# Optimization experiments

Measured on AMD Instinct MI355X. Metric: run time of the kernel, lower is better.

The kernel has to match this reference:

```python
import jax, jax.numpy as jnp
import numpy as np

N_NODES = 50000
N_EDGES = 500000
N_GRAPHS = 64
IN_DIM = 64
HID = 128
N_LAYERS = 2
BN_EPS = 1e-5


def setup_inputs() -> dict:
    key = jax.random.key(0)
    ks = jax.random.split(key, 12)
    x = jax.random.normal(ks[0], (N_NODES, IN_DIM), dtype=jnp.float32)
    edge_index = jax.random.randint(ks[1], (2, N_EDGES), 0, N_NODES, dtype=jnp.int64)
    batch = jnp.sort(jax.random.randint(ks[2], (N_NODES,), 0, N_GRAPHS, dtype=jnp.int64))
    s = 0.05
    W_enc = jax.random.normal(ks[3], (IN_DIM, HID), dtype=jnp.float32) * s
    b_enc = jnp.zeros((HID,), dtype=jnp.float32)
    Wc = jax.random.normal(ks[4], (N_LAYERS, HID, HID), dtype=jnp.float32) * s
    bc = jnp.zeros((N_LAYERS, HID), dtype=jnp.float32)
    gamma = jnp.ones((N_LAYERS, HID), dtype=jnp.float32)
    beta = jnp.zeros((N_LAYERS, HID), dtype=jnp.float32)
    MID = HID // 2
    W1 = jax.random.normal(ks[5], (HID, MID), dtype=jnp.float32) * s
    b1 = jnp.zeros((MID,), dtype=jnp.float32)
    W2 = jax.random.normal(ks[6], (MID, 1), dtype=jnp.float32) * s
    b2 = jnp.zeros((1,), dtype=jnp.float32)
    return {"x": x, "edge_index": edge_index, "batch": batch,
            "W_enc": W_enc, "b_enc": b_enc, "Wc": Wc, "bc": bc,
            "gamma": gamma, "beta": beta, "W1": W1, "b1": b1,
            "W2": W2, "b2": b2}


def _gcn_conv(h, src, dst, norm, W, b, n_nodes):
    # h: [N, HID]; src/dst: [E+N] (self-loops included); norm: [E+N]
    h = h @ W                                   # [N, HID]
    msg = h[src] * norm[:, None]                # gather + normalize
    out = jax.ops.segment_sum(msg, dst, num_segments=n_nodes)  # scatter-add
    return out + b


def _batch_norm(h, g, b):
    mu = jnp.mean(h, axis=0)
    var = jnp.var(h, axis=0)
    return (h - mu) * jax.lax.rsqrt(var + BN_EPS) * g + b


def reference(x, edge_index, batch, W_enc, b_enc, Wc, bc, gamma, beta, W1, b1, W2, b2):
    n = x.shape[0]
    loop = jnp.arange(n, dtype=edge_index.dtype)
    src = jnp.concatenate([edge_index[0], loop])   # [E+N]
    dst = jnp.concatenate([edge_index[1], loop])
    # symmetric GCN normalization with self-loops: deg over target index
    deg = jax.ops.segment_sum(jnp.ones_like(dst, dtype=x.dtype), dst, num_segments=n)
    dinv = jax.lax.rsqrt(deg)                      # deg >= 1 due to self-loops
    norm = dinv[src] * dinv[dst]                   # [E+N]

    h = x @ W_enc + b_enc                          # node encoder
    for l in range(Wc.shape[0]):
        h = _gcn_conv(h, src, dst, norm, Wc[l], bc[l], n)
        h = _batch_norm(h, gamma[l], beta[l])
        h = jax.nn.relu(h)                         # dropout inactive (eval)

    # global mean pool over graphs
    pooled = jax.ops.segment_sum(h, batch, num_segments=N_GRAPHS)
    counts = jax.ops.segment_sum(jnp.ones((n,), dtype=h.dtype), batch, num_segments=N_GRAPHS)
    pooled = pooled / jnp.maximum(counts, 1.0)[:, None]

    z = jax.nn.relu(pooled @ W1 + b1)
    out = jax.nn.sigmoid(z @ W2 + b2)              # [B, 1]
    return out.squeeze(-1)                          # [B]
```

## Files before the change

### kernel.cpp

```cpp
#include <hip/hip_runtime.h>
#include <hip/hip_bf16.h>
#include <hip/hip_fp16.h>
#include <math.h>


typedef _Float16 f16x8 __attribute__((ext_vector_type(8)));
typedef float f32x4 __attribute__((ext_vector_type(4)));

__device__ inline unsigned pack2(float a, float b) {
  union { __half2 h; unsigned u; } p;
  p.h = __floats2half2_rn(a, b);
  return p.u;
}
__device__ inline float2 unpack2(unsigned u) {
  union { unsigned u; __half2 h; } p;
  p.u = u;
  return __half22float2(p.h);
}

__global__ __launch_bounds__(256) void k_setup(
    int* __restrict__ deg, float* __restrict__ bnstat, int statTotal,
    float* __restrict__ pooled, int N, int nbN,
    const float* __restrict__ W_enc, const float* __restrict__ b_enc,
    const float* __restrict__ Wc, unsigned short* __restrict__ MT,
    float* __restrict__ bfold, int NL,
    const float* __restrict__ Wc1, unsigned short* __restrict__ WT1,
    const int* __restrict__ batch, int* __restrict__ gstart) {
  int b = blockIdx.x;
  if (b < nbN) {
    int i = b * 256 + threadIdx.x;
    if (i < N) deg[i] = 1;
    if (i < statTotal) bnstat[i] = 0.f;
    if (i < 64 * 128) pooled[i] = 0.f;
    return;
  }
  b -= nbN;
  if (b < 65) {
    if (threadIdx.x < 128) {
      int n = threadIdx.x;
      int k = b;
      const float* arow = (k < 64) ? (W_enc + (size_t)k * 128) : b_enc;
      float acc = 0.f;
      for (int j = 0; j < 128; j++)
        acc = fmaf(arow[j], Wc[(size_t)j * 128 + n], acc);
      if (k < 64) ((__half*)MT)[(size_t)n * 64 + k] = __float2half(acc);
      else bfold[n] = acc;
    }
    return;
  }
  b -= 65;
  if (b < 64) {
    if (NL > 1) {
      int i = b * 256 + threadIdx.x;
      int n = i & 127, k = i >> 7;
      ((__half*)WT1)[(size_t)n * 128 + k] = __float2half(Wc1[i]);
    }
    return;
  }
  int g = threadIdx.x;
  if (g <= 64) {
    int lo = 0, hi = N;
    while (lo < hi) {
      int mid = (lo + hi) >> 1;
      if (batch[mid] < g) lo = mid + 1;
      else hi = mid;
    }
    gstart[g] = lo;
  }
}

__global__ __launch_bounds__(256) void k_deg(const int* __restrict__ ei, int E,
                                             int* __restrict__ deg) {
  int i = blockIdx.x * 256 + threadIdx.x;
  if (i < E) atomicAdd(&deg[ei[E + i]], 1);
}

__global__ __launch_bounds__(256) void k_scan_a(const int* __restrict__ deg, int N,
                                                int* __restrict__ rowptr,
                                                int* __restrict__ blksum) {
  __shared__ int s[256];
  int t = threadIdx.x;
  int i = blockIdx.x * 256 + t;
  int v = (i < N) ? deg[i] : 0;
  s[t] = v;
  __syncthreads();
  for (int off = 1; off < 256; off <<= 1) {
    int x = (t >= off) ? s[t - off] : 0;
    __syncthreads();
    s[t] += x;
    __syncthreads();
  }
  if (i < N) rowptr[i] = s[t] - v;
  if (t == 255) blksum[blockIdx.x] = s[255];
}

__global__ __launch_bounds__(256) void k_scan_c(const int* __restrict__ deg, int N,
                                                int total,
                                                const int* __restrict__ blksum,
                                                int* __restrict__ rowptr,
                                                int* __restrict__ cursor,
                                                float* __restrict__ dinv) {
  __shared__ int red[256];
  int t = threadIdx.x, b = blockIdx.x;
  int acc = 0;
  for (int j = t; j < b; j += 256) acc += blksum[j];
  red[t] = acc;
  __syncthreads();
  for (int off = 128; off > 0; off >>= 1) {
    if (t < off) red[t] += red[t + off];
    __syncthreads();
  }
  int prefix = red[0];
  int i = b * 256 + t;
  if (i < N) {
    int rp = rowptr[i] + prefix;
    rowptr[i] = rp;
    cursor[i] = rp;
    dinv[i] = rsqrtf((float)deg[i]);
  } else if (i == N) {
    rowptr[N] = total;
  }
}

__global__ __launch_bounds__(256) void k_fillprep(
    const int* __restrict__ ei, int E, int N, int nbEN,
    int* __restrict__ cursor, int* __restrict__ colx,
    const float* __restrict__ x, const float* __restrict__ dinv,
    unsigned* __restrict__ xs2) {
  int b = blockIdx.x;
  if (b < nbEN) {
    int i = b * 256 + threadIdx.x;
    if (i < E) {
      int s = ei[i];
      int d = ei[E + i];
      int pos = atomicAdd(&cursor[d], 1);
      colx[pos] = s;
    } else if (i < E + N) {
      int j = i - E;
      int pos = atomicAdd(&cursor[j], 1);
      colx[pos] = j;
    }
    return;
  }
  b -= nbEN;
  int i = b * 256 + threadIdx.x;
  if (i < N * 16) {
    int row = i >> 4;
    float4 v = ((const float4*)x)[i];
    float d = dinv[row];
    uint2 o;
    o.x = pack2(v.x * d, v.y * d);
    o.y = pack2(v.z * d, v.w * d);
    ((uint2*)xs2)[i] = o;
  }
}

__global__ __launch_bounds__(256, 2) void k_aggemm0(
    const uint2* __restrict__ xs, const int* __restrict__ rowptr,
    const int* __restrict__ colx, const float* __restrict__ dinv,
    const unsigned short* __restrict__ MT,
    const float* __restrict__ bias,
    const float* __restrict__ bias2,
    float* __restrict__ stat,
    unsigned short* __restrict__ Yh, int N) {
  constexpr int KP = 68;
  __shared__ unsigned short Al[64 * KP];
  __shared__ float wvl[64];
  __shared__ float red[4][2][128];

  int lane = threadIdx.x & 63;
  int wv = threadIdx.x >> 6;
  int grp = lane >> 4, l16 = lane & 15;
  int rowBlk = blockIdx.x * 64;

#pragma unroll 1
  for (int it = 0; it < 4; it++) {
    int lr = it * 16 + wv * 4 + grp;
    int i = rowBlk + lr;
    float s0 = 0.f, s1 = 0.f, s2 = 0.f, s3 = 0.f, sd = 0.f;
    if (i < N) {
      int beg = rowptr[i], end = rowptr[i + 1];
      int e = beg;
#pragma unroll 1
      for (; e + 8 <= end; e += 8) {
        int ix[8];
#pragma unroll
        for (int u = 0; u < 8; u++) ix[u] = colx[e + u];
        uint2 v[8];
        float dd[8];
#pragma unroll
        for (int u = 0; u < 8; u++) { v[u] = xs[(size_t)ix[u] * 16 + l16]; dd[u] = dinv[ix[u]]; }
#pragma unroll
        for (int u = 0; u < 8; u++) {
          float2 a = unpack2(v[u].x), b = unpack2(v[u].y);
          s0 += a.x; s1 += a.y; s2 += b.x; s3 += b.y;
          sd += dd[u];
        }
      }
#pragma unroll 1
      for (; e < end; e++) {
        int sr = colx[e];
        uint2 vv = xs[(size_t)sr * 16 + l16];
        float2 a = unpack2(vv.x), b = unpack2(vv.y);
        s0 += a.x; s1 += a.y; s2 += b.x; s3 += b.y;
        sd += dinv[sr];
      }
    }
    float di = (i < N) ? dinv[i] : 0.f;
    *(uint2*)&Al[lr * KP + l16 * 4] =
        make_uint2(pack2(s0 * di, s1 * di), pack2(s2 * di, s3 * di));
    if (l16 == 0) wvl[lr] = di * sd;
  }
  __syncthreads();

  int l15 = lane & 15;
  int kg = lane >> 4;
  f16x8 af[2];
#pragma unroll
  for (int j = 0; j < 2; j++)
    af[j] = *(const f16x8*)&Al[(wv * 16 + l15) * KP + kg * 8 + j * 32];

  f32x4 acc[8];
#pragma unroll
  for (int t = 0; t < 8; t++) acc[t] = {0.f, 0.f, 0.f, 0.f};
#pragma unroll
  for (int j = 0; j < 2; j++) {
#pragma unroll
    for (int t = 0; t < 8; t++) {
      f16x8 bf = *(const f16x8*)&MT[(size_t)(t * 16 + l15) * 64 + kg * 8 + j * 32];
      acc[t] = __builtin_amdgcn_mfma_f32_16x16x32_f16(af[j], bf, acc[t], 0, 0, 0);
    }
  }

  int rbaseL = wv * 16 + kg * 4;
  int rbase = rowBlk + rbaseL;
  float wrow[4];
#pragma unroll
  for (int r = 0; r < 4; r++) wrow[r] = wvl[rbaseL + r];

#pragma unroll
  for (int t = 0; t < 8; t++) {
    int ch = t * 16 + l15;
    float bb = bias[ch];
    float b2v = bias2[ch];
    float s = 0.f, q = 0.f;
#pragma unroll
    for (int r = 0; r < 4; r++) {
      int row = rbase + r;
      if (row < N) {
        float o = fmaf(wrow[r], b2v, acc[t][r] + bb);
        __half oh = __float2half(o);
        Yh[(size_t)row * 128 + ch] = *(unsigned short*)&oh;
        s += o;
        q += o * o;
      }
    }
    s += __shfl_xor(s, 16); s += __shfl_xor(s, 32);
    q += __shfl_xor(q, 16); q += __shfl_xor(q, 32);
    if (kg == 0) { red[wv][0][ch] = s; red[wv][1][ch] = q; }
  }
  __syncthreads();
  int st = threadIdx.x >> 7, ch2 = threadIdx.x & 127;
  float v = red[0][st][ch2] + red[1][st][ch2] + red[2][st][ch2] + red[3][st][ch2];
  atomicAdd(&stat[(blockIdx.x & 7) * 256 + st * 128 + ch2], v);
}

__global__ __launch_bounds__(256, 2) void k_aggemm1(
    const unsigned short* __restrict__ Hprev,
    const int* __restrict__ rowptr, const int* __restrict__ colx,
    const float* __restrict__ dinv,
    const unsigned short* __restrict__ WT,
    const float* __restrict__ statPrev, const float* __restrict__ gamma,
    const float* __restrict__ beta, float invN,
    const float* __restrict__ bias,
    float* __restrict__ statCur, unsigned short* __restrict__ Yh, int N) {
  constexpr int KP = 136;
  __shared__ unsigned short Al[64 * KP];
  __shared__ float scsh[256];
  __shared__ float red[4][2][128];

  if (threadIdx.x < 128) {
    int c = threadIdx.x;
    float ss = 0.f, qs = 0.f;
#pragma unroll
    for (int r = 0; r < 8; r++) {
      ss += statPrev[r * 256 + c];
      qs += statPrev[r * 256 + 128 + c];
    }
    float mu = ss * invN;
    float var = qs * invN - mu * mu;
    float sc = rsqrtf(var + 1e-5f) * gamma[c];
    scsh[c] = sc;
    scsh[128 + c] = beta[c] - mu * sc;
  }
  __syncthreads();

  int lane = threadIdx.x & 63;
  int wv = threadIdx.x >> 6;
  int half = lane >> 5, l32 = lane & 31;
  int rowBlk = blockIdx.x * 64;
  const uint2* Hp = (const uint2*)Hprev;
  float4 sc = ((const float4*)scsh)[l32];
  float4 sh = ((const float4*)(scsh + 128))[l32];

#pragma unroll 1
  for (int it = 0; it < 8; it++) {
    int lr = it * 8 + wv * 2 + half;
    int i = rowBlk + lr;
    float4 s = make_float4(0.f, 0.f, 0.f, 0.f);
    if (i < N) {
      int beg = rowptr[i], end = rowptr[i + 1];
      int e = beg;
#pragma unroll 1
      for (; e + 4 <= end; e += 4) {
        int i0 = colx[e + 0], i1 = colx[e + 1], i2 = colx[e + 2], i3 = colx[e + 3];
        uint2 v0 = Hp[(size_t)i0 * 32 + l32];
        uint2 v1 = Hp[(size_t)i1 * 32 + l32];
        uint2 v2 = Hp[(size_t)i2 * 32 + l32];
        uint2 v3 = Hp[(size_t)i3 * 32 + l32];
        float d0 = dinv[i0], d1 = dinv[i1], d2 = dinv[i2], d3 = dinv[i3];
        float2 a, b;
        a = unpack2(v0.x); b = unpack2(v0.y);
        s.x += fmaxf(fmaf(a.x, sc.x, sh.x), 0.f) * d0;
        s.y += fmaxf(fmaf(a.y, sc.y, sh.y), 0.f) * d0;
        s.z += fmaxf(fmaf(b.x, sc.z, sh.z), 0.f) * d0;
        s.w += fmaxf(fmaf(b.y, sc.w, sh.w), 0.f) * d0;
        a = unpack2(v1.x); b = unpack2(v1.y);
        s.x += fmaxf(fmaf(a.x, sc.x, sh.x), 0.f) * d1;
        s.y += fmaxf(fmaf(a.y, sc.y, sh.y), 0.f) * d1;
        s.z += fmaxf(fmaf(b.x, sc.z, sh.z), 0.f) * d1;
        s.w += fmaxf(fmaf(b.y, sc.w, sh.w), 0.f) * d1;
        a = unpack2(v2.x); b = unpack2(v2.y);
        s.x += fmaxf(fmaf(a.x, sc.x, sh.x), 0.f) * d2;
        s.y += fmaxf(fmaf(a.y, sc.y, sh.y), 0.f) * d2;
        s.z += fmaxf(fmaf(b.x, sc.z, sh.z), 0.f) * d2;
        s.w += fmaxf(fmaf(b.y, sc.w, sh.w), 0.f) * d2;
        a = unpack2(v3.x); b = unpack2(v3.y);
        s.x += fmaxf(fmaf(a.x, sc.x, sh.x), 0.f) * d3;
        s.y += fmaxf(fmaf(a.y, sc.y, sh.y), 0.f) * d3;
        s.z += fmaxf(fmaf(b.x, sc.z, sh.z), 0.f) * d3;
        s.w += fmaxf(fmaf(b.y, sc.w, sh.w), 0.f) * d3;
      }
#pragma unroll 1
      for (; e < end; e++) {
        int sr = colx[e];
        uint2 vv = Hp[(size_t)sr * 32 + l32];
        float dsr = dinv[sr];
        float2 a = unpack2(vv.x), b = unpack2(vv.y);
        s.x += fmaxf(fmaf(a.x, sc.x, sh.x), 0.f) * dsr;
        s.y += fmaxf(fmaf(a.y, sc.y, sh.y), 0.f) * dsr;
        s.z += fmaxf(fmaf(b.x, sc.z, sh.z), 0.f) * dsr;
        s.w += fmaxf(fmaf(b.y, sc.w, sh.w), 0.f) * dsr;
      }
    }
    float di = (i < N) ? dinv[i] : 0.f;
    *(uint2*)&Al[lr * KP + l32 * 4] =
        make_uint2(pack2(s.x * di, s.y * di), pack2(s.z * di, s.w * di));
  }
  __syncthreads();

  int l15 = lane & 15;
  int kg = lane >> 4;
  f16x8 af[4];
#pragma unroll
  for (int j = 0; j < 4; j++)
    af[j] = *(const f16x8*)&Al[(wv * 16 + l15) * KP + kg * 8 + j * 32];

  f32x4 acc[8];
#pragma unroll
  for (int t = 0; t < 8; t++) acc[t] = {0.f, 0.f, 0.f, 0.f};
#pragma unroll
  for (int j = 0; j < 4; j++) {
#pragma unroll
    for (int t = 0; t < 8; t++) {
      f16x8 bf = *(const f16x8*)&WT[(size_t)(t * 16 + l15) * 128 + kg * 8 + j * 32];
      acc[t] = __builtin_amdgcn_mfma_f32_16x16x32_f16(af[j], bf, acc[t], 0, 0, 0);
    }
  }

  int rbase = rowBlk + wv * 16 + kg * 4;
#pragma unroll
  for (int t = 0; t < 8; t++) {
    int ch = t * 16 + l15;
    float bb = bias[ch];
    float s = 0.f, q = 0.f;
#pragma unroll
    for (int r = 0; r < 4; r++) {
      int row = rbase + r;
      if (row < N) {
        float o = acc[t][r] + bb;
        __half oh = __float2half(o);
        Yh[(size_t)row * 128 + ch] = *(unsigned short*)&oh;
        s += o;
        q += o * o;
      }
    }
    s += __shfl_xor(s, 16); s += __shfl_xor(s, 32);
    q += __shfl_xor(q, 16); q += __shfl_xor(q, 32);
    if (kg == 0) { red[wv][0][ch] = s; red[wv][1][ch] = q; }
  }
  __syncthreads();
  int st = threadIdx.x >> 7, ch2 = threadIdx.x & 127;
  float v = red[0][st][ch2] + red[1][st][ch2] + red[2][st][ch2] + red[3][st][ch2];
  atomicAdd(&statCur[(blockIdx.x & 7) * 256 + st * 128 + ch2], v);
}

__global__ __launch_bounds__(256) void k_wprep(const float* __restrict__ Wsrc,
                                               unsigned short* __restrict__ WT) {
  int i = blockIdx.x * 256 + threadIdx.x;
  int n = i & 127, k = i >> 7;
  ((__half*)WT)[(size_t)n * 128 + k] = __float2half(Wsrc[i]);
}

__global__ __launch_bounds__(256) void k_pool(
    const unsigned* __restrict__ H16u,
    const float* __restrict__ stat, const float* __restrict__ gamma,
    const float* __restrict__ beta, float invN,
    const int* __restrict__ gstart, float* __restrict__ pooled) {
  __shared__ float scsh[256];
  __shared__ float red[4][128];
  if (threadIdx.x < 128) {
    int c = threadIdx.x;
    float ss = 0.f, qs = 0.f;
#pragma unroll
    for (int r = 0; r < 8; r++) {
      ss += stat[r * 256 + c];
      qs += stat[r * 256 + 128 + c];
    }
    float mu = ss * invN;
    float var = qs * invN - mu * mu;
    float sc = rsqrtf(var + 1e-5f) * gamma[c];
    scsh[c] = sc;
    scsh[128 + c] = beta[c] - mu * sc;
  }
  __syncthreads();

  int g = blockIdx.x >> 3;
  int part = blockIdx.x & 7;
  int beg = gstart[g], end = gstart[g + 1];
  int len = end - beg;
  int p0 = beg + (len * part) / 8;
  int p1 = beg + (len * (part + 1)) / 8;

  int l64 = threadIdx.x & 63;
  int rs = threadIdx.x >> 6;
  int c0 = l64 * 2;
  float sc0 = scsh[c0], sc1 = scsh[c0 + 1];
  float sh0 = scsh[128 + c0], sh1 = scsh[128 + c0 + 1];
  int plen = p1 - p0;
  int q0 = p0 + (plen * rs) / 4;
  int q1 = p0 + (plen * (rs + 1)) / 4;

  float a0 = 0.f, a1 = 0.f;
  for (int r = q0; r < q1; r++) {
    float2 f = unpack2(H16u[(size_t)r * 64 + l64]);
    a0 += fmaxf(fmaf(f.x, sc0, sh0), 0.f);
    a1 += fmaxf(fmaf(f.y, sc1, sh1), 0.f);
  }
  red[rs][c0] = a0;
  red[rs][c0 + 1] = a1;
  __syncthreads();
  if (threadIdx.x < 128) {
    float s = red[0][threadIdx.x] + red[1][threadIdx.x] +
              red[2][threadIdx.x] + red[3][threadIdx.x];
    atomicAdd(&pooled[g * 128 + threadIdx.x], s);
  }
}

__global__ __launch_bounds__(256) void k_mlp(const float* __restrict__ pooled,
                                             const int* __restrict__ gstart,
                                             const float* __restrict__ W1,
                                             const float* __restrict__ b1,
                                             const float* __restrict__ W2,
                                             const float* __restrict__ b2,
                                             float* __restrict__ out) {
  __shared__ float P[64 * 128];
  __shared__ float Z[64 * 64];
  for (int i = threadIdx.x; i < 64 * 128; i += 256) {
    int g = i >> 7;
    int cnt = gstart[g + 1] - gstart[g];
    P[i] = pooled[i] / (float)(cnt > 1 ? cnt : 1);
  }
  __syncthreads();
  for (int i = threadIdx.x; i < 64 * 64; i += 256) {
    int g = i >> 6, m = i & 63;
    float acc = b1[m];
    for (int k = 0; k < 128; k++) acc += P[(g << 7) + k] * W1[k * 64 + m];
    Z[i] = fmaxf(acc, 0.f);
  }
  __syncthreads();
  if (threadIdx.x < 64) {
    int g = threadIdx.x;
    float acc = b2[0];
    for (int m = 0; m < 64; m++) acc += Z[(g << 6) + m] * W2[m];
    out[g] = 1.f / (1.f + expf(-acc));
  }
}


extern "C" void kernel_launch(void* const* d_in, const int* in_sizes, int n_in,
                              void* d_out, int out_size, void* d_ws, size_t ws_size,
                              hipStream_t stream) {
  const float* x      = (const float*)d_in[0];
  const int*   ei     = (const int*)d_in[1];
  const int*   batch  = (const int*)d_in[2];
  const float* W_enc  = (const float*)d_in[3];
  const float* b_enc  = (const float*)d_in[4];
  const float* Wc     = (const float*)d_in[5];
  const float* bc     = (const float*)d_in[6];
  const float* gamma  = (const float*)d_in[7];
  const float* beta   = (const float*)d_in[8];
  const float* W1     = (const float*)d_in[9];
  const float* b1     = (const float*)d_in[10];
  const float* W2     = (const float*)d_in[11];
  const float* b2     = (const float*)d_in[12];
  float* out = (float*)d_out;

  const int N = in_sizes[2];
  const int E = in_sizes[1] / 2;
  const int NL = in_sizes[6] / 128;

  size_t off = 0;
  auto alloc = [&](size_t bytes) {
    void* p = (char*)d_ws + off;
    off += (bytes + 255) & ~(size_t)255;
    return p;
  };
  unsigned short* h16a = (unsigned short*)alloc((size_t)N * 128 * 2);
  unsigned short* h16b = (unsigned short*)alloc((size_t)N * 128 * 2);
  int*   deg    = (int*)alloc((size_t)N * 4);
  float* dinv   = (float*)alloc((size_t)N * 4);
  int*   rowptr = (int*)alloc((size_t)(N + 1) * 4);
  int*   cursor = (int*)alloc((size_t)N * 4);
  int*   colx   = (int*)alloc((size_t)(E + N) * 4);
  int*   blksum = (int*)alloc(1024 * 4);
  float* bnstat = (float*)alloc((size_t)NL * 2048 * 4);
  float* pooled = (float*)alloc(64 * 128 * 4);
  int*   gstart = (int*)alloc(65 * 4);
  unsigned short* MT  = (unsigned short*)alloc(128 * 64 * 2);
  unsigned short* WT1 = (unsigned short*)alloc(128 * 128 * 2);
  float* bfold  = (float*)alloc(128 * 4);
  unsigned* xs  = (unsigned*)alloc((size_t)N * 64 * 2);

  int nbN = (N + 255) / 256;
  int nbEN = (E + N + 255) / 256;
  float invN = 1.f / (float)N;
  int tiles = (N + 63) / 64;

  k_setup<<<nbN + 130, 256, 0, stream>>>(
      deg, bnstat, NL * 2048, pooled, N, nbN, W_enc, b_enc, Wc, MT, bfold, NL,
      Wc + (size_t)128 * 128, WT1, batch, gstart);
  k_deg<<<(E + 255) / 256, 256, 0, stream>>>(ei, E, deg);
  k_scan_a<<<nbN, 256, 0, stream>>>(deg, N, rowptr, blksum);
  k_scan_c<<<nbN, 256, 0, stream>>>(deg, N, E + N, blksum, rowptr, cursor, dinv);
  k_fillprep<<<nbEN + (N * 16 + 255) / 256, 256, 0, stream>>>(
      ei, E, N, nbEN, cursor, colx, x, dinv, xs);

  k_aggemm0<<<tiles, 256, 0, stream>>>((const uint2*)xs, rowptr, colx, dinv,
                                       MT, bc, bfold, bnstat, h16a, N);

  unsigned short* cur = h16a;
  unsigned short* nxt = h16b;
  for (int l = 1; l < NL; l++) {
    if (l > 1)
      k_wprep<<<64, 256, 0, stream>>>(Wc + (size_t)l * 128 * 128, WT1);
    k_aggemm1<<<tiles, 256, 0, stream>>>(
        cur, rowptr, colx, dinv, WT1, bnstat + (l - 1) * 2048,
        gamma + (l - 1) * 128, beta + (l - 1) * 128, invN, bc + l * 128,
        bnstat + l * 2048, nxt, N);
    unsigned short* tmp = cur; cur = nxt; nxt = tmp;
  }

  k_pool<<<64 * 8, 256, 0, stream>>>((const unsigned*)cur,
                                     bnstat + (NL - 1) * 2048,
                                     gamma + (NL - 1) * 128,
                                     beta + (NL - 1) * 128, invN, gstart,
                                     pooled);
  k_mlp<<<1, 256, 0, stream>>>(pooled, gstart, W1, b1, W2, b2, out);
}
```

Measured before the change: 282.7 us.

## Halve row tiles to 32, split GEMM over 2x2 waves, unroll gather by 8

Both fused aggregate+GEMM kernels now process 32 rows per block instead of 64. The four waves split the MFMA output as 2 row-halves by 2 column-halves, so each wave keeps 4 accumulators instead of 8. Launch bounds are raised to 4 blocks per SM to allow more waves in flight for the latency-bound neighbor gather. The layer-1 gather loop is unrolled to 8 edges for more memory-level parallelism. The grid doubles, which adds more per-block BN-stat atomics and more redundant weight-fragment reads per row.

After: 258.5 us. -8.6%, faster.

```diff
diff --git a/kernel.cpp b/kernel.cpp
--- a/kernel.cpp
+++ b/kernel.cpp
@@ -155,7 +155,7 @@
   }
 }
 
-__global__ __launch_bounds__(256, 2) void k_aggemm0(
+__global__ __launch_bounds__(256, 4) void k_aggemm0(
     const uint2* __restrict__ xs, const int* __restrict__ rowptr,
     const int* __restrict__ colx, const float* __restrict__ dinv,
     const unsigned short* __restrict__ MT,
@@ -164,17 +164,17 @@
     float* __restrict__ stat,
     unsigned short* __restrict__ Yh, int N) {
   constexpr int KP = 68;
-  __shared__ unsigned short Al[64 * KP];
-  __shared__ float wvl[64];
-  __shared__ float red[4][2][128];
+  __shared__ unsigned short Al[32 * KP];
+  __shared__ float wvl[32];
+  __shared__ float red[2][2][128];
 
   int lane = threadIdx.x & 63;
   int wv = threadIdx.x >> 6;
   int grp = lane >> 4, l16 = lane & 15;
-  int rowBlk = blockIdx.x * 64;
+  int rowBlk = blockIdx.x * 32;
 
 #pragma unroll 1
-  for (int it = 0; it < 4; it++) {
+  for (int it = 0; it < 2; it++) {
     int lr = it * 16 + wv * 4 + grp;
     int i = rowBlk + lr;
     float s0 = 0.f, s1 = 0.f, s2 = 0.f, s3 = 0.f, sd = 0.f;
@@ -215,32 +215,33 @@
 
   int l15 = lane & 15;
   int kg = lane >> 4;
+  int wr = wv & 1, wc = wv >> 1;
   f16x8 af[2];
 #pragma unroll
   for (int j = 0; j < 2; j++)
-    af[j] = *(const f16x8*)&Al[(wv * 16 + l15) * KP + kg * 8 + j * 32];
-
-  f32x4 acc[8];
-#pragma unroll
-  for (int t = 0; t < 8; t++) acc[t] = {0.f, 0.f, 0.f, 0.f};
+    af[j] = *(const f16x8*)&Al[(wr * 16 + l15) * KP + kg * 8 + j * 32];
+
+  f32x4 acc[4];
+#pragma unroll
+  for (int t = 0; t < 4; t++) acc[t] = {0.f, 0.f, 0.f, 0.f};
 #pragma unroll
   for (int j = 0; j < 2; j++) {
 #pragma unroll
-    for (int t = 0; t < 8; t++) {
-      f16x8 bf = *(const f16x8*)&MT[(size_t)(t * 16 + l15) * 64 + kg * 8 + j * 32];
+    for (int t = 0; t < 4; t++) {
+      f16x8 bf = *(const f16x8*)&MT[(size_t)(wc * 64 + t * 16 + l15) * 64 + kg * 8 + j * 32];
       acc[t] = __builtin_amdgcn_mfma_f32_16x16x32_f16(af[j], bf, acc[t], 0, 0, 0);
     }
   }
 
-  int rbaseL = wv * 16 + kg * 4;
+  int rbaseL = wr * 16 + kg * 4;
   int rbase = rowBlk + rbaseL;
   float wrow[4];
 #pragma unroll
   for (int r = 0; r < 4; r++) wrow[r] = wvl[rbaseL + r];
 
 #pragma unroll
-  for (int t = 0; t < 8; t++) {
-    int ch = t * 16 + l15;
+  for (int t = 0; t < 4; t++) {
+    int ch = wc * 64 + t * 16 + l15;
     float bb = bias[ch];
     float b2v = bias2[ch];
     float s = 0.f, q = 0.f;
@@ -257,15 +258,15 @@
     }
     s += __shfl_xor(s, 16); s += __shfl_xor(s, 32);
     q += __shfl_xor(q, 16); q += __shfl_xor(q, 32);
-    if (kg == 0) { red[wv][0][ch] = s; red[wv][1][ch] = q; }
+    if (kg == 0) { red[wr][0][ch] = s; red[wr][1][ch] = q; }
   }
   __syncthreads();
   int st = threadIdx.x >> 7, ch2 = threadIdx.x & 127;
-  float v = red[0][st][ch2] + red[1][st][ch2] + red[2][st][ch2] + red[3][st][ch2];
+  float v = red[0][st][ch2] + red[1][st][ch2];
   atomicAdd(&stat[(blockIdx.x & 7) * 256 + st * 128 + ch2], v);
 }
 
-__global__ __launch_bounds__(256, 2) void k_aggemm1(
+__global__ __launch_bounds__(256, 4) void k_aggemm1(
     const unsigned short* __restrict__ Hprev,
     const int* __restrict__ rowptr, const int* __restrict__ colx,
     const float* __restrict__ dinv,
@@ -275,9 +276,9 @@
     const float* __restrict__ bias,
     float* __restrict__ statCur, unsigned short* __restrict__ Yh, int N) {
   constexpr int KP = 136;
-  __shared__ unsigned short Al[64 * KP];
+  __shared__ unsigned short Al[32 * KP];
   __shared__ float scsh[256];
-  __shared__ float red[4][2][128];
+  __shared__ float red[2][2][128];
 
   if (threadIdx.x < 128) {
     int c = threadIdx.x;
@@ -298,13 +299,13 @@
   int lane = threadIdx.x & 63;
   int wv = threadIdx.x >> 6;
   int half = lane >> 5, l32 = lane & 31;
-  int rowBlk = blockIdx.x * 64;
+  int rowBlk = blockIdx.x * 32;
   const uint2* Hp = (const uint2*)Hprev;
   float4 sc = ((const float4*)scsh)[l32];
   float4 sh = ((const float4*)(scsh + 128))[l32];
 
 #pragma unroll 1
-  for (int it = 0; it < 8; it++) {
+  for (int it = 0; it < 4; it++) {
     int lr = it * 8 + wv * 2 + half;
     int i = rowBlk + lr;
     float4 s = make_float4(0.f, 0.f, 0.f, 0.f);
@@ -312,34 +313,22 @@
       int beg = rowptr[i], end = rowptr[i + 1];
       int e = beg;
 #pragma unroll 1
-      for (; e + 4 <= end; e += 4) {
-        int i0 = colx[e + 0], i1 = colx[e + 1], i2 = colx[e + 2], i3 = colx[e + 3];
-        uint2 v0 = Hp[(size_t)i0 * 32 + l32];
-        uint2 v1 = Hp[(size_t)i1 * 32 + l32];
-        uint2 v2 = Hp[(size_t)i2 * 32 + l32];
-        uint2 v3 = Hp[(size_t)i3 * 32 + l32];
-        float d0 = dinv[i0], d1 = dinv[i1], d2 = dinv[i2], d3 = dinv[i3];
-        float2 a, b;
-        a = unpack2(v0.x); b = unpack2(v0.y);
-        s.x += fmaxf(fmaf(a.x, sc.x, sh.x), 0.f) * d0;
-        s.y += fmaxf(fmaf(a.y, sc.y, sh.y), 0.f) * d0;
-        s.z += fmaxf(fmaf(b.x, sc.z, sh.z), 0.f) * d0;
-        s.w += fmaxf(fmaf(b.y, sc.w, sh.w), 0.f) * d0;
-        a = unpack2(v1.x); b = unpack2(v1.y);
-        s.x += fmaxf(fmaf(a.x, sc.x, sh.x), 0.f) * d1;
-        s.y += fmaxf(fmaf(a.y, sc.y, sh.y), 0.f) * d1;
-        s.z += fmaxf(fmaf(b.x, sc.z, sh.z), 0.f) * d1;
-        s.w += fmaxf(fmaf(b.y, sc.w, sh.w), 0.f) * d1;
-        a = unpack2(v2.x); b = unpack2(v2.y);
-        s.x += fmaxf(fmaf(a.x, sc.x, sh.x), 0.f) * d2;
-        s.y += fmaxf(fmaf(a.y, sc.y, sh.y), 0.f) * d2;
-        s.z += fmaxf(fmaf(b.x, sc.z, sh.z), 0.f) * d2;
-        s.w += fmaxf(fmaf(b.y, sc.w, sh.w), 0.f) * d2;
-        a = unpack2(v3.x); b = unpack2(v3.y);
-        s.x += fmaxf(fmaf(a.x, sc.x, sh.x), 0.f) * d3;
-        s.y += fmaxf(fmaf(a.y, sc.y, sh.y), 0.f) * d3;
-        s.z += fmaxf(fmaf(b.x, sc.z, sh.z), 0.f) * d3;
-        s.w += fmaxf(fmaf(b.y, sc.w, sh.w), 0.f) * d3;
+      for (; e + 8 <= end; e += 8) {
+        int ix[8];
+#pragma unroll
+        for (int u = 0; u < 8; u++) ix[u] = colx[e + u];
+        uint2 v[8];
+        float dd[8];
+#pragma unroll
+        for (int u = 0; u < 8; u++) { v[u] = Hp[(size_t)ix[u] * 32 + l32]; dd[u] = dinv[ix[u]]; }
+#pragma unroll
+        for (int u = 0; u < 8; u++) {
+          float2 a = unpack2(v[u].x), b = unpack2(v[u].y);
+          s.x += fmaxf(fmaf(a.x, sc.x, sh.x), 0.f) * dd[u];
+          s.y += fmaxf(fmaf(a.y, sc.y, sh.y), 0.f) * dd[u];
+          s.z += fmaxf(fmaf(b.x, sc.z, sh.z), 0.f) * dd[u];
+          s.w += fmaxf(fmaf(b.y, sc.w, sh.w), 0.f) * dd[u];
+        }
       }
 #pragma unroll 1
       for (; e < end; e++) {
@@ -361,27 +350,28 @@
 
   int l15 = lane & 15;
   int kg = lane >> 4;
+  int wr = wv & 1, wc = wv >> 1;
   f16x8 af[4];
 #pragma unroll
   for (int j = 0; j < 4; j++)
-    af[j] = *(const f16x8*)&Al[(wv * 16 + l15) * KP + kg * 8 + j * 32];
-
-  f32x4 acc[8];
-#pragma unroll
-  for (int t = 0; t < 8; t++) acc[t] = {0.f, 0.f, 0.f, 0.f};
+    af[j] = *(const f16x8*)&Al[(wr * 16 + l15) * KP + kg * 8 + j * 32];
+
+  f32x4 acc[4];
+#pragma unroll
+  for (int t = 0; t < 4; t++) acc[t] = {0.f, 0.f, 0.f, 0.f};
 #pragma unroll
   for (int j = 0; j < 4; j++) {
 #pragma unroll
-    for (int t = 0; t < 8; t++) {
-      f16x8 bf = *(const f16x8*)&WT[(size_t)(t * 16 + l15) * 128 + kg * 8 + j * 32];
+    for (int t = 0; t < 4; t++) {
+      f16x8 bf = *(const f16x8*)&WT[(size_t)(wc * 64 + t * 16 + l15) * 128 + kg * 8 + j * 32];
       acc[t] = __builtin_amdgcn_mfma_f32_16x16x32_f16(af[j], bf, acc[t], 0, 0, 0);
     }
   }
 
-  int rbase = rowBlk + wv * 16 + kg * 4;
-#pragma unroll
-  for (int t = 0; t < 8; t++) {
-    int ch = t * 16 + l15;
+  int rbase = rowBlk + wr * 16 + kg * 4;
+#pragma unroll
+  for (int t = 0; t < 4; t++) {
+    int ch = wc * 64 + t * 16 + l15;
     float bb = bias[ch];
     float s = 0.f, q = 0.f;
 #pragma unroll
@@ -397,11 +387,11 @@
     }
     s += __shfl_xor(s, 16); s += __shfl_xor(s, 32);
     q += __shfl_xor(q, 16); q += __shfl_xor(q, 32);
-    if (kg == 0) { red[wv][0][ch] = s; red[wv][1][ch] = q; }
+    if (kg == 0) { red[wr][0][ch] = s; red[wr][1][ch] = q; }
   }
   __syncthreads();
   int st = threadIdx.x >> 7, ch2 = threadIdx.x & 127;
-  float v = red[0][st][ch2] + red[1][st][ch2] + red[2][st][ch2] + red[3][st][ch2];
+  float v = red[0][st][ch2] + red[1][st][ch2];
   atomicAdd(&statCur[(blockIdx.x & 7) * 256 + st * 128 + ch2], v);
 }
 
@@ -545,7 +535,7 @@
   int nbN = (N + 255) / 256;
   int nbEN = (E + N + 255) / 256;
   float invN = 1.f / (float)N;
-  int tiles = (N + 63) / 64;
+  int tiles32 = (N + 31) / 32;
 
   k_setup<<<nbN + 130, 256, 0, stream>>>(
       deg, bnstat, NL * 2048, pooled, N, nbN, W_enc, b_enc, Wc, MT, bfold, NL,
@@ -556,15 +546,15 @@
   k_fillprep<<<nbEN + (N * 16 + 255) / 256, 256, 0, stream>>>(
       ei, E, N, nbEN, cursor, colx, x, dinv, xs);
 
-  k_aggemm0<<<tiles, 256, 0, stream>>>((const uint2*)xs, rowptr, colx, dinv,
-                                       MT, bc, bfold, bnstat, h16a, N);
+  k_aggemm0<<<tiles32, 256, 0, stream>>>((const uint2*)xs, rowptr, colx, dinv,
+                                         MT, bc, bfold, bnstat, h16a, N);
 
   unsigned short* cur = h16a;
   unsigned short* nxt = h16b;
   for (int l = 1; l < NL; l++) {
     if (l > 1)
       k_wprep<<<64, 256, 0, stream>>>(Wc + (size_t)l * 128 * 128, WT1);
-    k_aggemm1<<<tiles, 256, 0, stream>>>(
+    k_aggemm1<<<tiles32, 256, 0, stream>>>(
         cur, rowptr, colx, dinv, WT1, bnstat + (l - 1) * 2048,
         gamma + (l - 1) * 128, beta + (l - 1) * 128, invN, bc + l * 128,
         bnstat + l * 2048, nxt, N);
```
